# Optimization experiments

Hardware: AMD Instinct MI355X
Metric: run time of the kernel (lower is better)

## Reference

```python
import jax, jax.numpy as jnp
import numpy as np

B, T = 256, 512
V, E, H = 82, 256, 128  # vocab, embedding_dim, hidden_size (hardcoded in ckpt consts)


def setup_inputs() -> dict:
    key = jax.random.key(0)
    ks = jax.random.split(key, 12)
    sqrt_k = (1.0 / H) ** 0.5
    sqrt_kc = (1.0 / H) ** 0.5  # nn.Linear(H, V) default init scale

    def u(k, shape, s):
        return jax.random.uniform(k, shape, minval=-s, maxval=s, dtype=jnp.float32)

    emb = jax.random.normal(ks[0], (V, E), dtype=jnp.float32) * 0.1
    emb = emb.at[0].set(0.0)  # padding_idx=0
    W_f = u(ks[1], (H, 2 * H + E), sqrt_k)
    W_i = u(ks[2], (H, 2 * H + E), sqrt_k)
    W_o = u(ks[3], (H, 2 * H + E), sqrt_k)
    W_c = u(ks[4], (H, H + E), sqrt_k)
    b_f = u(ks[5], (H,), sqrt_k)
    b_i = u(ks[6], (H,), sqrt_k)
    b_o = u(ks[7], (H,), sqrt_k)
    b_c = u(ks[8], (H,), sqrt_k)
    W_cls = u(ks[9], (V, H), sqrt_kc)
    b_cls = u(ks[10], (V,), sqrt_kc)
    batch_reviews = jax.random.randint(ks[11], (B, T), 0, V, dtype=jnp.int32)
    return {"batch_reviews": batch_reviews, "emb": emb,
            "W_f": W_f, "W_i": W_i, "W_o": W_o, "W_c": W_c,
            "b_f": b_f, "b_i": b_i, "b_o": b_o, "b_c": b_c,
            "W_cls": W_cls, "b_cls": b_cls}


def reference(batch_reviews, emb, W_f, W_i, W_o, W_c, b_f, b_i, b_o, b_c, W_cls, b_cls):
    x = emb[batch_reviews]              # [B, T, E]
    xs = jnp.swapaxes(x, 0, 1)          # [T, B, E] for scan over time
    h0 = jnp.zeros((x.shape[0], H), dtype=x.dtype)
    c0 = jnp.zeros((x.shape[0], H), dtype=x.dtype)

    def step(carry, xt):
        h, c = carry
        chx = jnp.concatenate([c, h, xt], axis=1)   # [B, 2H+E]
        hx = jnp.concatenate([h, xt], axis=1)       # [B, H+E]
        f = jax.nn.sigmoid(chx @ W_f.T + b_f)
        i = jax.nn.sigmoid(chx @ W_i.T + b_i)
        o = jax.nn.sigmoid(chx @ W_o.T + b_o)
        c_tilde = jnp.tanh(hx @ W_c.T + b_c)
        next_c = f * c + i * c_tilde
        next_h = o * jnp.tanh(next_c)
        return (next_h, next_c), (f, i, o)

    (h, c), (f_all, i_all, o_all) = jax.lax.scan(step, (h0, c0), xs)
    logits = h @ W_cls.T + b_cls        # classifier on final hidden state
    return logits, f_all, i_all, o_all  # gates stacked [T, B, H]
```

## Files before the change

kernel.cpp:

```cpp
#include <hip/hip_runtime.h>


typedef __bf16 bf16;
typedef __bf16 bf16x4 __attribute__((ext_vector_type(4)));
typedef __bf16 bf16x8 __attribute__((ext_vector_type(8)));
typedef float  f32x4  __attribute__((ext_vector_type(4)));

#define NB 256
#define NT 512
#define NV 82
#define NE 256
#define NH 128

#define MFMA16(a, b, c) __builtin_amdgcn_mfma_f32_16x16x32_bf16((a), (b), (c), 0, 0, 0)

__device__ __forceinline__ float sigf(float x) {
    return __builtin_amdgcn_rcpf(1.f + __expf(-x));
}
__device__ __forceinline__ float tanhf_(float x) {
    return fmaf(-2.f, __builtin_amdgcn_rcpf(1.f + __expf(2.f * x)), 1.f);
}

__device__ __forceinline__ bool data_is_bf16(const void* emb) {
    const unsigned short* u = (const unsigned short*)emb;
    int cnt = 0;
    for (int i = 512; i < 768; ++i) {
        int e = (u[i] >> 7) & 0xFF;
        cnt += (e >= 97 && e <= 126) ? 1 : 0;
    }
    return cnt >= 200;
}

__device__ __forceinline__ bf16x8 load8(const bf16* p) { return *(const bf16x8*)p; }
__device__ __forceinline__ bf16x8 load8(const float* p) {
    f32x4 a = *(const f32x4*)p;
    f32x4 b = *(const f32x4*)(p + 4);
    bf16x8 r;
    r[0] = (bf16)a[0]; r[1] = (bf16)a[1]; r[2] = (bf16)a[2]; r[3] = (bf16)a[3];
    r[4] = (bf16)b[0]; r[5] = (bf16)b[1]; r[6] = (bf16)b[2]; r[7] = (bf16)b[3];
    return r;
}

template <typename T>
__global__ __launch_bounds__(256, 1) void k_xproj(
    const int* __restrict__ tok, const T* __restrict__ emb,
    const T* __restrict__ Wf, const T* __restrict__ Wi, const T* __restrict__ Wo,
    const T* __restrict__ Bf, const T* __restrict__ Bi, const T* __restrict__ Bo,
    char* __restrict__ gf, char* __restrict__ gi, char* __restrict__ go)
{
    if (data_is_bf16(emb) != (sizeof(T) == 2)) return;

    const size_t TS = (size_t)32768 * sizeof(T);
    const size_t BS = (size_t)2048 * sizeof(T);

    const int lane = threadIdx.x & 63;
    const int wave = threadIdx.x >> 6;
    const int l15  = lane & 15;
    const int q8   = (lane >> 4) * 8;

    const int mt4 = blockIdx.x;
    const int t   = mt4 >> 2;
    const int b0  = (mt4 & 3) * 64;
    const int ht  = blockIdx.y * 4 + wave;
    const int h   = ht * 16 + l15;

    const T* wf = Wf + h * 512 + 256 + q8;
    const T* wi = Wi + h * 512 + 256 + q8;
    const T* wo = Wo + h * 512 + 256 + q8;

    const T* arow[4];
#pragma unroll
    for (int s = 0; s < 4; ++s) {
        int b  = b0 + s * 16 + l15;
        int tk = tok[b * NT + t];
        arow[s] = emb + (size_t)tk * NE + q8;
    }

    const float vF = (float)Bf[h], vI = (float)Bi[h], vO = (float)Bo[h];
    f32x4 aF[4], aI[4], aO[4];
#pragma unroll
    for (int s = 0; s < 4; ++s) {
        aF[s] = f32x4{vF, vF, vF, vF};
        aI[s] = f32x4{vI, vI, vI, vI};
        aO[s] = f32x4{vO, vO, vO, vO};
    }

#pragma unroll
    for (int k = 0; k < NE; k += 32) {
        bf16x8 bF = load8(wf + k);
        bf16x8 bI = load8(wi + k);
        bf16x8 bO = load8(wo + k);
#pragma unroll
        for (int s = 0; s < 4; ++s) {
            bf16x8 a = load8(arow[s] + k);
            aF[s] = MFMA16(a, bF, aF[s]);
            aI[s] = MFMA16(a, bI, aI[s]);
            aO[s] = MFMA16(a, bO, aO[s]);
        }
    }

#pragma unroll
    for (int s = 0; s < 4; ++s) {
        int bg = (b0 >> 4) + s;
        size_t off = (size_t)t * TS + (size_t)bg * BS + (size_t)(ht * 512 + lane * 8);
        bf16x4 o4;
        o4[0] = (bf16)aF[s][0]; o4[1] = (bf16)aF[s][1]; o4[2] = (bf16)aF[s][2]; o4[3] = (bf16)aF[s][3];
        *(bf16x4*)(gf + off) = o4;
        o4[0] = (bf16)aI[s][0]; o4[1] = (bf16)aI[s][1]; o4[2] = (bf16)aI[s][2]; o4[3] = (bf16)aI[s][3];
        *(bf16x4*)(gi + off) = o4;
        o4[0] = (bf16)aO[s][0]; o4[1] = (bf16)aO[s][1]; o4[2] = (bf16)aO[s][2]; o4[3] = (bf16)aO[s][3];
        *(bf16x4*)(go + off) = o4;
    }
}

template <typename T>
__global__ __launch_bounds__(512, 1) void k_recur(
    const int* __restrict__ tok, const T* __restrict__ emb,
    const T* __restrict__ Wf, const T* __restrict__ Wi,
    const T* __restrict__ Wo, const T* __restrict__ Wc,
    const T* __restrict__ Bc,
    const T* __restrict__ Wcls, const T* __restrict__ Bcls,
    char* __restrict__ gf, char* __restrict__ gi, char* __restrict__ go,
    T* __restrict__ out)
{
    if (data_is_bf16(emb) != (sizeof(T) == 2)) return;

    const size_t TS = (size_t)32768 * sizeof(T);
    const size_t BS = (size_t)2048 * sizeof(T);

    __shared__ __align__(16) bf16 cb[2][16][136];
    __shared__ __align__(16) bf16 hb[2][16][136];
    __shared__ int   ltok[16][516];
    __shared__ float hfp[16][128];

    const int tid  = threadIdx.x;
    const int lane = tid & 63;
    const int ht   = tid >> 6;
    const int l15  = lane & 15;
    const int quad = lane >> 4;
    const int q8   = quad * 8;
    const int bg   = blockIdx.x;
    const int h    = ht * 16 + l15;

    {
        bf16* cp = &cb[0][0][0];
        bf16* hp = &hb[0][0][0];
        for (int i = tid; i < 2 * 16 * 136; i += 512) { cp[i] = (bf16)0.f; hp[i] = (bf16)0.f; }
        for (int i = tid; i < 16 * 512; i += 512) {
            int r = i >> 9, t = i & 511;
            ltok[r][t] = tok[(bg * 16 + r) * NT + t];
        }
    }
    __syncthreads();

    bf16x8 Wfc[4], Wic[4], Woc[4];
    bf16x8 Wfh[4], Wih[4], Woh[4];
    bf16x8 Wch[4];
    bf16x8 Wcx[8];
    {
        const T* pf = Wf + h * 512 + q8;
        const T* pi = Wi + h * 512 + q8;
        const T* po = Wo + h * 512 + q8;
        const T* pc = Wc + h * 384 + q8;
#pragma unroll
        for (int j = 0; j < 4; ++j) {
            Wfc[j] = load8(pf + j * 32);
            Wic[j] = load8(pi + j * 32);
            Woc[j] = load8(po + j * 32);
            Wfh[j] = load8(pf + 128 + j * 32);
            Wih[j] = load8(pi + 128 + j * 32);
            Woh[j] = load8(po + 128 + j * 32);
            Wch[j] = load8(pc + j * 32);
        }
#pragma unroll
        for (int j = 0; j < 8; ++j) Wcx[j] = load8(pc + 128 + j * 32);
    }

    const float vC = (float)Bc[h];
    f32x4 creg = {0.f, 0.f, 0.f, 0.f};

    const size_t cbase = (size_t)bg * BS + (size_t)(ht * 512 + lane * 8);
    bf16x4 xf = *(const bf16x4*)(gf + cbase);
    bf16x4 xi = *(const bf16x4*)(gi + cbase);
    bf16x4 xo = *(const bf16x4*)(go + cbase);

    for (int t = 0; t < NT; ++t) {
        const int rb = t & 1, wb = rb ^ 1;

        f32x4 aF = {(float)xf[0], (float)xf[1], (float)xf[2], (float)xf[3]};
        f32x4 aI = {(float)xi[0], (float)xi[1], (float)xi[2], (float)xi[3]};
        f32x4 aO = {(float)xo[0], (float)xo[1], (float)xo[2], (float)xo[3]};
        f32x4 aC = {vC, vC, vC, vC};

#pragma unroll
        for (int j = 0; j < 4; ++j) {
            bf16x8 a = *(const bf16x8*)(&cb[rb][l15][j * 32 + q8]);
            aF = MFMA16(a, Wfc[j], aF);
            aI = MFMA16(a, Wic[j], aI);
            aO = MFMA16(a, Woc[j], aO);
        }
#pragma unroll
        for (int j = 0; j < 4; ++j) {
            bf16x8 a = *(const bf16x8*)(&hb[rb][l15][j * 32 + q8]);
            aF = MFMA16(a, Wfh[j], aF);
            aI = MFMA16(a, Wih[j], aI);
            aO = MFMA16(a, Woh[j], aO);
            aC = MFMA16(a, Wch[j], aC);
        }
        {
            int tk = ltok[l15][t];
            const T* xr = emb + (size_t)tk * NE + q8;
#pragma unroll
            for (int j = 0; j < 8; ++j) aC = MFMA16(load8(xr + j * 32), Wcx[j], aC);
        }

        {
            size_t nidx = (size_t)((t < NT - 1) ? t + 1 : t) * TS + cbase;
            xf = *(const bf16x4*)(gf + nidx);
            xi = *(const bf16x4*)(gi + nidx);
            xo = *(const bf16x4*)(go + nidx);
        }

        const size_t ob = (size_t)t * TS + (size_t)bg * BS + (size_t)h * sizeof(T);
#pragma unroll
        for (int r = 0; r < 4; ++r) {
            const int row = quad * 4 + r;
            float fv = sigf(aF[r]);
            float iv = sigf(aI[r]);
            float ov = sigf(aO[r]);
            float cv = tanhf_(aC[r]);
            float cn = fv * creg[r] + iv * cv;
            float hn = ov * tanhf_(cn);
            creg[r] = cn;
            cb[wb][row][h] = (bf16)cn;
            hb[wb][row][h] = (bf16)hn;
            size_t o = ob + (size_t)row * (128 * sizeof(T));
            *(T*)(gf + o) = (T)fv;
            *(T*)(gi + o) = (T)iv;
            *(T*)(go + o) = (T)ov;
            if (t == NT - 1) hfp[row][h] = hn;
        }
        __syncthreads();
    }

    for (int idx = tid; idx < 16 * NV; idx += 512) {
        int row = idx / NV;
        int v   = idx - row * NV;
        float acc = (float)Bcls[v];
        const T* wr = Wcls + v * NH;
        float s = 0.f;
#pragma unroll 4
        for (int k = 0; k < NH; ++k) s += hfp[row][k] * (float)wr[k];
        out[(size_t)(bg * 16 + row) * NV + v] = (T)(acc + s);
    }
}

#define TS4 ((size_t)131072)
#define BS4 ((size_t)8192)
#define NTILES ((NB * NT) / 64)
#define ELDS 264

__global__ __launch_bounds__(512, 2) void k_xproj6(
    const int* __restrict__ tok, const float* __restrict__ emb,
    const float* __restrict__ Wf, const float* __restrict__ Wi,
    const float* __restrict__ Wo, const float* __restrict__ Wc,
    const float* __restrict__ Bf, const float* __restrict__ Bi,
    const float* __restrict__ Bo, const float* __restrict__ Bc,
    char* __restrict__ gf, char* __restrict__ gi, char* __restrict__ go)
{
    if (data_is_bf16(emb)) return;

    __shared__ __align__(16) bf16 eL[NV][ELDS];

    const int tid  = threadIdx.x;
    const int lane = tid & 63;
    const int wv   = tid >> 6;
    const int l15  = lane & 15;
    const int q8   = (lane >> 4) * 8;
    const int ht   = wv;
    const int h    = ht * 16 + l15;

    for (int i = tid; i < (NV * NE) / 4; i += 512) {
        int e0 = i * 4;
        int r  = e0 >> 8;
        int c  = e0 & (NE - 1);
        f32x4 v = *(const f32x4*)(emb + e0);
        bf16x4 w;
        w[0] = (bf16)v[0]; w[1] = (bf16)v[1]; w[2] = (bf16)v[2]; w[3] = (bf16)v[3];
        *(bf16x4*)(&eL[r][c]) = w;
    }
    __syncthreads();

    auto run_gate = [&](const float* wrow, float bias,
                        char* dst, size_t extra) __attribute__((always_inline)) {
        bf16x8 W[8];
#pragma unroll
        for (int j = 0; j < 8; ++j) W[j] = load8(wrow + j * 32);

        for (int tile = blockIdx.x; tile < NTILES; tile += 256) {
            const int t  = tile >> 2;
            const int b0 = (tile & 3) * 64;

            int tk[4];
#pragma unroll
            for (int s = 0; s < 4; ++s)
                tk[s] = tok[(b0 + s * 16 + l15) * NT + t];

            f32x4 acc[4];
#pragma unroll
            for (int s = 0; s < 4; ++s) acc[s] = f32x4{bias, bias, bias, bias};

#pragma unroll
            for (int j = 0; j < 8; ++j) {
                const int k = j * 32;
#pragma unroll
                for (int s = 0; s < 4; ++s) {
                    bf16x8 a = *(const bf16x8*)(&eL[tk[s]][k + q8]);
                    acc[s] = MFMA16(a, W[j], acc[s]);
                }
            }

#pragma unroll
            for (int s = 0; s < 4; ++s) {
                int bg = (b0 >> 4) + s;
                size_t off = (size_t)t * TS4 + (size_t)bg * BS4
                           + (size_t)(ht * 512 + lane * 8) + extra;
                bf16x4 o4;
                o4[0] = (bf16)acc[s][0]; o4[1] = (bf16)acc[s][1];
                o4[2] = (bf16)acc[s][2]; o4[3] = (bf16)acc[s][3];
                *(bf16x4*)(dst + off) = o4;
            }
        }
    };

    run_gate(Wf + h * 512 + 256 + q8, Bf[h], gf, 0);
    run_gate(Wi + h * 512 + 256 + q8, Bi[h], gi, 0);
    run_gate(Wo + h * 512 + 256 + q8, Bo[h], go, 0);
    run_gate(Wc + h * 384 + 128 + q8, Bc[h], gi, 4096);
}

struct GState {
    f32x4  creg;
    bf16x4 xf, xi, xo, xc;
};

__device__ __forceinline__ void lstm_step2(
    bf16 (*__restrict__ cb)[16][136], bf16 (*__restrict__ hb)[16][136],
    const bf16x8* Wfc, const bf16x8* Wic, const bf16x8* Woc,
    const bf16x8* Wfh, const bf16x8* Wih, const bf16x8* Woh,
    const bf16x8* Wch,
    GState& g,
    char* __restrict__ gf, char* __restrict__ gi, char* __restrict__ go,
    size_t cbase, size_t gb, int t, int rb, int wb,
    int l15, int quad, int q8, int h, float (*__restrict__ hp)[128])
{
    f32x4 aF = {(float)g.xf[0], (float)g.xf[1], (float)g.xf[2], (float)g.xf[3]};
    f32x4 aI = {(float)g.xi[0], (float)g.xi[1], (float)g.xi[2], (float)g.xi[3]};
    f32x4 aO = {(float)g.xo[0], (float)g.xo[1], (float)g.xo[2], (float)g.xo[3]};
    f32x4 aC = {(float)g.xc[0], (float)g.xc[1], (float)g.xc[2], (float)g.xc[3]};

#pragma unroll
    for (int j = 0; j < 4; ++j) {
        bf16x8 a = *(const bf16x8*)(&cb[rb][l15][j * 32 + q8]);
        aF = MFMA16(a, Wfc[j], aF);
        aI = MFMA16(a, Wic[j], aI);
        aO = MFMA16(a, Woc[j], aO);
    }
#pragma unroll
    for (int j = 0; j < 4; ++j) {
        bf16x8 a = *(const bf16x8*)(&hb[rb][l15][j * 32 + q8]);
        aF = MFMA16(a, Wfh[j], aF);
        aI = MFMA16(a, Wih[j], aI);
        aO = MFMA16(a, Woh[j], aO);
        aC = MFMA16(a, Wch[j], aC);
    }

    {
        size_t nidx = (size_t)((t < NT - 1) ? t + 1 : t) * TS4 + cbase;
        g.xf = *(const bf16x4*)(gf + nidx);
        g.xi = *(const bf16x4*)(gi + nidx);
        g.xo = *(const bf16x4*)(go + nidx);
        g.xc = *(const bf16x4*)(gi + nidx + 4096);
    }

    const size_t ob = (size_t)t * TS4 + gb;
#pragma unroll
    for (int r = 0; r < 4; ++r) {
        const int row = quad * 4 + r;
        float fv = sigf(aF[r]);
        float iv = sigf(aI[r]);
        float ov = sigf(aO[r]);
        float cv = tanhf_(aC[r]);
        float cn = fv * g.creg[r] + iv * cv;
        float hn = ov * tanhf_(cn);
        g.creg[r] = cn;
        cb[wb][row][h] = (bf16)cn;
        hb[wb][row][h] = (bf16)hn;
        size_t o = ob + (size_t)(row * 512);
        *(float*)(gf + o) = fv;
        *(float*)(gi + o) = iv;
        *(float*)(go + o) = ov;
        if (t == NT - 1) hp[row][h] = hn;
    }
}

__global__ __launch_bounds__(512, 1) void k_recur2(
    const float* __restrict__ emb,
    const float* __restrict__ Wf, const float* __restrict__ Wi,
    const float* __restrict__ Wo, const float* __restrict__ Wc,
    const float* __restrict__ Wcls, const float* __restrict__ Bcls,
    char* __restrict__ gf, char* __restrict__ gi, char* __restrict__ go,
    float* __restrict__ out)
{
    if (data_is_bf16(emb)) return;

    __shared__ __align__(16) bf16 cb[2][16][136];
    __shared__ __align__(16) bf16 hb[2][16][136];
    __shared__ __align__(16) float hfp[16][128];

    const int tid  = threadIdx.x;
    const int lane = tid & 63;
    const int ht   = tid >> 6;
    const int l15  = lane & 15;
    const int quad = lane >> 4;
    const int q8   = quad * 8;
    const int bg   = blockIdx.x;
    const int h    = ht * 16 + l15;

    {
        bf16* cp = &cb[0][0][0];
        bf16* hp = &hb[0][0][0];
        for (int i = tid; i < 2 * 16 * 136; i += 512) { cp[i] = (bf16)0.f; hp[i] = (bf16)0.f; }
    }

    bf16x8 Wfc[4], Wic[4], Woc[4], Wfh[4], Wih[4], Woh[4], Wch[4];
    {
        const float* pf = Wf + h * 512 + q8;
        const float* pi = Wi + h * 512 + q8;
        const float* po = Wo + h * 512 + q8;
        const float* pc = Wc + h * 384 + q8;
#pragma unroll
        for (int j = 0; j < 4; ++j) {
            Wfc[j] = load8(pf + j * 32);
            Wic[j] = load8(pi + j * 32);
            Woc[j] = load8(po + j * 32);
            Wfh[j] = load8(pf + 128 + j * 32);
            Wih[j] = load8(pi + 128 + j * 32);
            Woh[j] = load8(po + 128 + j * 32);
            Wch[j] = load8(pc + j * 32);
        }
    }

    GState A;
    A.creg = f32x4{0.f, 0.f, 0.f, 0.f};

    const size_t cbase = (size_t)bg * BS4 + (size_t)(ht * 512 + lane * 8);
    const size_t gb    = (size_t)bg * BS4 + (size_t)h * 4;

    A.xf = *(const bf16x4*)(gf + cbase);
    A.xi = *(const bf16x4*)(gi + cbase);
    A.xo = *(const bf16x4*)(go + cbase);
    A.xc = *(const bf16x4*)(gi + cbase + 4096);

    __syncthreads();

    for (int t = 0; t < NT; ++t) {
        const int rb = t & 1, wb = rb ^ 1;

        lstm_step2(cb, hb, Wfc, Wic, Woc, Wfh, Wih, Woh, Wch,
                   A, gf, gi, go, cbase, gb, t, rb, wb, l15, quad, q8, h, hfp);

        asm volatile("s_waitcnt vmcnt(12) lgkmcnt(0)" ::: "memory");
        __builtin_amdgcn_sched_barrier(0);
        __builtin_amdgcn_s_barrier();
        __builtin_amdgcn_sched_barrier(0);
    }

    for (int idx = tid; idx < 16 * NV; idx += 512) {
        int row = idx / NV;
        int v   = idx - row * NV;
        float acc = Bcls[v];
        const float* wr = Wcls + v * NH;
        float s = 0.f;
#pragma unroll 4
        for (int k = 0; k < NH; ++k) s += hfp[row][k] * wr[k];
        out[(size_t)(bg * 16 + row) * NV + v] = acc + s;
    }
}

template <typename T>
static void launch_all(void* const* d_in, void* d_out, hipStream_t stream)
{
    const int* tok = (const int*)d_in[0];
    const T* emb  = (const T*)d_in[1];
    const T* Wf   = (const T*)d_in[2];
    const T* Wi   = (const T*)d_in[3];
    const T* Wo   = (const T*)d_in[4];
    const T* Wc   = (const T*)d_in[5];
    const T* Bf   = (const T*)d_in[6];
    const T* Bi   = (const T*)d_in[7];
    const T* Bo   = (const T*)d_in[8];
    const T* Bc   = (const T*)d_in[9];
    const T* Wcls = (const T*)d_in[10];
    const T* Bcls = (const T*)d_in[11];

    char* gf = (char*)d_out + (size_t)NB * NV * sizeof(T);
    char* gi = gf + (size_t)NT * NB * NH * sizeof(T);
    char* go = gi + (size_t)NT * NB * NH * sizeof(T);

    k_xproj<T><<<dim3((NB * NT) / 64, 2), 256, 0, stream>>>(
        tok, emb, Wf, Wi, Wo, Bf, Bi, Bo, gf, gi, go);
    k_recur<T><<<dim3(16), 512, 0, stream>>>(
        tok, emb, Wf, Wi, Wo, Wc, Bc, Wcls, Bcls, gf, gi, go, (T*)d_out);
}

static void launch_f32(void* const* d_in, void* d_out, hipStream_t stream)
{
    const int* tok     = (const int*)d_in[0];
    const float* emb   = (const float*)d_in[1];
    const float* Wf    = (const float*)d_in[2];
    const float* Wi    = (const float*)d_in[3];
    const float* Wo    = (const float*)d_in[4];
    const float* Wc    = (const float*)d_in[5];
    const float* Bf    = (const float*)d_in[6];
    const float* Bi    = (const float*)d_in[7];
    const float* Bo    = (const float*)d_in[8];
    const float* Bc    = (const float*)d_in[9];
    const float* Wcls  = (const float*)d_in[10];
    const float* Bcls  = (const float*)d_in[11];

    char* gf = (char*)d_out + (size_t)NB * NV * sizeof(float);
    char* gi = gf + (size_t)NT * NB * NH * sizeof(float);
    char* go = gi + (size_t)NT * NB * NH * sizeof(float);

    k_xproj6<<<dim3(256), 512, 0, stream>>>(
        tok, emb, Wf, Wi, Wo, Wc, Bf, Bi, Bo, Bc, gf, gi, go);
    k_recur2<<<dim3(16), 512, 0, stream>>>(
        emb, Wf, Wi, Wo, Wc, Wcls, Bcls, gf, gi, go, (float*)d_out);
}

extern "C" void kernel_launch(void* const* d_in, const int* in_sizes, int n_in,
                              void* d_out, int out_size, void* d_ws, size_t ws_size,
                              hipStream_t stream)
{
    launch_f32(d_in, d_out, stream);
    launch_all<bf16>(d_in, d_out, stream);
}
```

Measured before the change: 977.3 us.

## Precompute per-vocab input projection table and gather it inside the recurrence

Because the vocabulary has only 82 tokens, the input-side gate projections (emb @ W_x + bias) are precomputed once per vocab entry into a small bf16 table in workspace. The recurrence kernel then gathers the table row for the next token each step, replacing the large per-(batch,time) x-projection kernel that wrote and reread a full T×B×H staging buffer. This cuts a large amount of compute and memory traffic, but adds dependent gather loads, with the token id read from LDS, inside the serial time loop. The new path is used only when the workspace is large enough.

After: 902.3 us. -7.7%, faster.

```diff
diff --git a/kernel.cpp b/kernel.cpp
--- a/kernel.cpp
+++ b/kernel.cpp
@@ -260,6 +260,205 @@
 #define NTILES ((NB * NT) / 64)
 #define ELDS 264
 
+__global__ __launch_bounds__(512, 1) void k_table(
+    const float* __restrict__ emb,
+    const float* __restrict__ Wf, const float* __restrict__ Wi,
+    const float* __restrict__ Wo, const float* __restrict__ Wc,
+    const float* __restrict__ Bf, const float* __restrict__ Bi,
+    const float* __restrict__ Bo, const float* __restrict__ Bc,
+    bf16* __restrict__ tbl)
+{
+    if (data_is_bf16(emb)) return;
+
+    const int tid  = threadIdx.x;
+    const int lane = tid & 63;
+    const int ht   = tid >> 6;
+    const int l15  = lane & 15;
+    const int quad = lane >> 4;
+    const int q8   = quad * 8;
+    const int h    = ht * 16 + l15;
+
+    const int vbase = blockIdx.x * 16;
+    const int va    = min(vbase + l15, NV - 1);
+    const float* erow = emb + (size_t)va * NE + q8;
+
+    const float* wrows[4] = {
+        Wf + h * 512 + 256 + q8,
+        Wi + h * 512 + 256 + q8,
+        Wo + h * 512 + 256 + q8,
+        Wc + h * 384 + 128 + q8
+    };
+    const float biases[4] = { Bf[h], Bi[h], Bo[h], Bc[h] };
+
+#pragma unroll
+    for (int g = 0; g < 4; ++g) {
+        const float b = biases[g];
+        f32x4 acc = {b, b, b, b};
+#pragma unroll
+        for (int j = 0; j < 8; ++j)
+            acc = MFMA16(load8(erow + j * 32), load8(wrows[g] + j * 32), acc);
+#pragma unroll
+        for (int r = 0; r < 4; ++r) {
+            int vo = vbase + quad * 4 + r;
+            if (vo < NV) tbl[(size_t)vo * 512 + h * 4 + g] = (bf16)acc[r];
+        }
+    }
+}
+
+__device__ __forceinline__ void lstm_step5(
+    bf16 (*__restrict__ cb)[16][136], bf16 (*__restrict__ hb)[16][136],
+    const bf16x8* Wfc, const bf16x8* Wic, const bf16x8* Woc,
+    const bf16x8* Wfh, const bf16x8* Wih, const bf16x8* Woh,
+    const bf16x8* Wch,
+    f32x4& creg, bf16x4* __restrict__ xq,
+    const bf16* __restrict__ tbl, const int (*__restrict__ ltok)[516],
+    char* __restrict__ gf, char* __restrict__ gi, char* __restrict__ go,
+    size_t gb, int t, int rb, int wb,
+    int l15, int quad, int q8, int h, float (*__restrict__ hp)[128])
+{
+    f32x4 aF = {(float)xq[0][0], (float)xq[1][0], (float)xq[2][0], (float)xq[3][0]};
+    f32x4 aI = {(float)xq[0][1], (float)xq[1][1], (float)xq[2][1], (float)xq[3][1]};
+    f32x4 aO = {(float)xq[0][2], (float)xq[1][2], (float)xq[2][2], (float)xq[3][2]};
+    f32x4 aC = {(float)xq[0][3], (float)xq[1][3], (float)xq[2][3], (float)xq[3][3]};
+
+#pragma unroll
+    for (int j = 0; j < 4; ++j) {
+        bf16x8 a = *(const bf16x8*)(&cb[rb][l15][j * 32 + q8]);
+        aF = MFMA16(a, Wfc[j], aF);
+        aI = MFMA16(a, Wic[j], aI);
+        aO = MFMA16(a, Woc[j], aO);
+    }
+#pragma unroll
+    for (int j = 0; j < 4; ++j) {
+        bf16x8 a = *(const bf16x8*)(&hb[rb][l15][j * 32 + q8]);
+        aF = MFMA16(a, Wfh[j], aF);
+        aI = MFMA16(a, Wih[j], aI);
+        aO = MFMA16(a, Woh[j], aO);
+        aC = MFMA16(a, Wch[j], aC);
+    }
+
+    {
+        const int tn = (t < NT - 1) ? t + 1 : t;
+#pragma unroll
+        for (int r = 0; r < 4; ++r) {
+            int tk = ltok[quad * 4 + r][tn];
+            xq[r] = *(const bf16x4*)(tbl + (size_t)tk * 512 + h * 4);
+        }
+    }
+
+    const size_t ob = (size_t)t * TS4 + gb;
+#pragma unroll
+    for (int r = 0; r < 4; ++r) {
+        const int row = quad * 4 + r;
+        float fv = sigf(aF[r]);
+        float iv = sigf(aI[r]);
+        float ov = sigf(aO[r]);
+        float cv = tanhf_(aC[r]);
+        float cn = fv * creg[r] + iv * cv;
+        float hn = ov * tanhf_(cn);
+        creg[r] = cn;
+        cb[wb][row][h] = (bf16)cn;
+        hb[wb][row][h] = (bf16)hn;
+        size_t o = ob + (size_t)(row * 512);
+        *(float*)(gf + o) = fv;
+        *(float*)(gi + o) = iv;
+        *(float*)(go + o) = ov;
+        if (t == NT - 1) hp[row][h] = hn;
+    }
+}
+
+__global__ __launch_bounds__(512, 1) void k_recur3(
+    const int* __restrict__ tok, const float* __restrict__ emb,
+    const float* __restrict__ Wf, const float* __restrict__ Wi,
+    const float* __restrict__ Wo, const float* __restrict__ Wc,
+    const float* __restrict__ Wcls, const float* __restrict__ Bcls,
+    const bf16* __restrict__ tbl,
+    char* __restrict__ gf, char* __restrict__ gi, char* __restrict__ go,
+    float* __restrict__ out)
+{
+    if (data_is_bf16(emb)) return;
+
+    __shared__ __align__(16) bf16 cb[2][16][136];
+    __shared__ __align__(16) bf16 hb[2][16][136];
+    __shared__ int   ltok[16][516];
+    __shared__ __align__(16) float hfp[16][128];
+
+    const int tid  = threadIdx.x;
+    const int lane = tid & 63;
+    const int ht   = tid >> 6;
+    const int l15  = lane & 15;
+    const int quad = lane >> 4;
+    const int q8   = quad * 8;
+    const int bg   = blockIdx.x;
+    const int h    = ht * 16 + l15;
+
+    {
+        bf16* cp = &cb[0][0][0];
+        bf16* hp = &hb[0][0][0];
+        for (int i = tid; i < 2 * 16 * 136; i += 512) { cp[i] = (bf16)0.f; hp[i] = (bf16)0.f; }
+        for (int i = tid; i < 16 * 512; i += 512) {
+            int r = i >> 9, t = i & 511;
+            ltok[r][t] = tok[(bg * 16 + r) * NT + t];
+        }
+    }
+
+    bf16x8 Wfc[4], Wic[4], Woc[4], Wfh[4], Wih[4], Woh[4], Wch[4];
+    {
+        const float* pf = Wf + h * 512 + q8;
+        const float* pi = Wi + h * 512 + q8;
+        const float* po = Wo + h * 512 + q8;
+        const float* pc = Wc + h * 384 + q8;
+#pragma unroll
+        for (int j = 0; j < 4; ++j) {
+            Wfc[j] = load8(pf + j * 32);
+            Wic[j] = load8(pi + j * 32);
+            Woc[j] = load8(po + j * 32);
+            Wfh[j] = load8(pf + 128 + j * 32);
+            Wih[j] = load8(pi + 128 + j * 32);
+            Woh[j] = load8(po + 128 + j * 32);
+            Wch[j] = load8(pc + j * 32);
+        }
+    }
+
+    f32x4 creg = {0.f, 0.f, 0.f, 0.f};
+    const size_t gb = (size_t)bg * BS4 + (size_t)h * 4;
+
+    __syncthreads();
+
+    bf16x4 xq[4];
+#pragma unroll
+    for (int r = 0; r < 4; ++r) {
+        int tk = ltok[quad * 4 + r][0];
+        xq[r] = *(const bf16x4*)(tbl + (size_t)tk * 512 + h * 4);
+    }
+
+    __syncthreads();
+
+    for (int t = 0; t < NT; ++t) {
+        const int rb = t & 1, wb = rb ^ 1;
+
+        lstm_step5(cb, hb, Wfc, Wic, Woc, Wfh, Wih, Woh, Wch,
+                   creg, xq, tbl, ltok, gf, gi, go, gb, t, rb, wb,
+                   l15, quad, q8, h, hfp);
+
+        asm volatile("s_waitcnt vmcnt(12) lgkmcnt(0)" ::: "memory");
+        __builtin_amdgcn_sched_barrier(0);
+        __builtin_amdgcn_s_barrier();
+        __builtin_amdgcn_sched_barrier(0);
+    }
+
+    for (int idx = tid; idx < 16 * NV; idx += 512) {
+        int row = idx / NV;
+        int v   = idx - row * NV;
+        float acc = Bcls[v];
+        const float* wr = Wcls + v * NH;
+        float s = 0.f;
+#pragma unroll 4
+        for (int k = 0; k < NH; ++k) s += hfp[row][k] * wr[k];
+        out[(size_t)(bg * 16 + row) * NV + v] = acc + s;
+    }
+}
+
 __global__ __launch_bounds__(512, 2) void k_xproj6(
     const int* __restrict__ tok, const float* __restrict__ emb,
     const float* __restrict__ Wf, const float* __restrict__ Wi,
@@ -466,10 +665,8 @@
 
     for (int t = 0; t < NT; ++t) {
         const int rb = t & 1, wb = rb ^ 1;
-
         lstm_step2(cb, hb, Wfc, Wic, Woc, Wfh, Wih, Woh, Wch,
                    A, gf, gi, go, cbase, gb, t, rb, wb, l15, quad, q8, h, hfp);
-
         asm volatile("s_waitcnt vmcnt(12) lgkmcnt(0)" ::: "memory");
         __builtin_amdgcn_sched_barrier(0);
         __builtin_amdgcn_s_barrier();
@@ -514,7 +711,8 @@
         tok, emb, Wf, Wi, Wo, Wc, Bc, Wcls, Bcls, gf, gi, go, (T*)d_out);
 }
 
-static void launch_f32(void* const* d_in, void* d_out, hipStream_t stream)
+static void launch_f32(void* const* d_in, void* d_out, void* d_ws, size_t ws_size,
+                       hipStream_t stream)
 {
     const int* tok     = (const int*)d_in[0];
     const float* emb   = (const float*)d_in[1];
@@ -533,16 +731,25 @@
     char* gi = gf + (size_t)NT * NB * NH * sizeof(float);
     char* go = gi + (size_t)NT * NB * NH * sizeof(float);
 
-    k_xproj6<<<dim3(256), 512, 0, stream>>>(
-        tok, emb, Wf, Wi, Wo, Wc, Bf, Bi, Bo, Bc, gf, gi, go);
-    k_recur2<<<dim3(16), 512, 0, stream>>>(
-        emb, Wf, Wi, Wo, Wc, Wcls, Bcls, gf, gi, go, (float*)d_out);
+    const size_t tbl_bytes = (size_t)NV * 512 * sizeof(bf16);
+    if (d_ws != nullptr && ws_size >= tbl_bytes) {
+        bf16* tbl = (bf16*)d_ws;
+        k_table<<<dim3(6), 512, 0, stream>>>(
+            emb, Wf, Wi, Wo, Wc, Bf, Bi, Bo, Bc, tbl);
+        k_recur3<<<dim3(16), 512, 0, stream>>>(
+            tok, emb, Wf, Wi, Wo, Wc, Wcls, Bcls, tbl, gf, gi, go, (float*)d_out);
+    } else {
+        k_xproj6<<<dim3(256), 512, 0, stream>>>(
+            tok, emb, Wf, Wi, Wo, Wc, Bf, Bi, Bo, Bc, gf, gi, go);
+        k_recur2<<<dim3(16), 512, 0, stream>>>(
+            emb, Wf, Wi, Wo, Wc, Wcls, Bcls, gf, gi, go, (float*)d_out);
+    }
 }
 
 extern "C" void kernel_launch(void* const* d_in, const int* in_sizes, int n_in,
                               void* d_out, int out_size, void* d_ws, size_t ws_size,
                               hipStream_t stream)
 {
-    launch_f32(d_in, d_out, stream);
+    launch_f32(d_in, d_out, d_ws, ws_size, stream);
     launch_all<bf16>(d_in, d_out, stream);
 }
```
